# Kernel optimization log

Hardware: AMD Instinct MI355X
Metric: run time of the kernel (lower is better)

The kernel has to match this reference:

```python
import jax, jax.numpy as jnp
import numpy as np

D_MODEL = 1024
D_STATE = 16
D_CONV = 4
EXPAND = 2
D_INNER = D_MODEL * EXPAND
LN_EPS = 1e-5


def setup_inputs() -> dict:
    key = jax.random.key(0)
    ks = jax.random.split(key, 12)
    s = lambda fan_in: 1.0 / np.sqrt(fan_in)
    return {
        "x": jax.random.normal(ks[0], (4, 2048, D_MODEL), dtype=jnp.float32),
        "ln_w": jnp.ones((D_MODEL,), jnp.float32),
        "ln_b": jnp.zeros((D_MODEL,), jnp.float32),
        "W_in": jax.random.uniform(ks[1], (D_MODEL, 2 * D_INNER), jnp.float32, -s(D_MODEL), s(D_MODEL)),
        "b_in": jax.random.uniform(ks[2], (2 * D_INNER,), jnp.float32, -s(D_MODEL), s(D_MODEL)),
        "conv_w": jax.random.uniform(ks[3], (D_INNER, 1, D_CONV), jnp.float32, -s(D_CONV), s(D_CONV)),
        "conv_b": jax.random.uniform(ks[4], (D_INNER,), jnp.float32, -s(D_CONV), s(D_CONV)),
        "A_log": jax.random.normal(ks[5], (D_INNER, D_STATE), jnp.float32),
        "D": jax.random.normal(ks[6], (D_INNER,), jnp.float32),
        "W_x": jax.random.uniform(ks[7], (D_INNER, 2 * D_STATE), jnp.float32, -s(D_INNER), s(D_INNER)),
        "b_x": jax.random.uniform(ks[8], (2 * D_STATE,), jnp.float32, -s(D_INNER), s(D_INNER)),
        "W_out": jax.random.uniform(ks[9], (D_INNER, D_MODEL), jnp.float32, -s(D_INNER), s(D_INNER)),
        "b_out": jax.random.uniform(ks[10], (D_MODEL,), jnp.float32, -s(D_INNER), s(D_INNER)),
    }


def _selective_scan(xc, deltaA, Bm, Cm):
    # xc: (b, s, di), deltaA: (di, n), Bm/Cm: (b, s, n)
    b, _, di = xc.shape
    n = Bm.shape[-1]
    h0 = jnp.zeros((b, di, n), xc.dtype)

    def step(h, inp):
        xt, bt, ct = inp  # (b,di), (b,n), (b,n)
        h = deltaA[None] * h + xt[:, :, None] * bt[:, None, :]
        y = jnp.einsum('bin,bn->bi', h, ct)
        return h, y

    xs = (jnp.swapaxes(xc, 0, 1), jnp.swapaxes(Bm, 0, 1), jnp.swapaxes(Cm, 0, 1))
    _, ys = jax.lax.scan(step, h0, xs)  # ys: (s, b, di)
    return jnp.swapaxes(ys, 0, 1)


def reference(x, ln_w, ln_b, W_in, b_in, conv_w, conv_b, A_log, D, W_x, b_x, W_out, b_out):
    residual = x
    mu = jnp.mean(x, -1, keepdims=True)
    var = jnp.mean((x - mu) ** 2, -1, keepdims=True)
    xn = (x - mu) * jax.lax.rsqrt(var + LN_EPS) * ln_w + ln_b
    xg = xn @ W_in + b_in
    x_main, gate = jnp.split(xg, 2, axis=-1)  # (b,s,di) each
    # causal depthwise conv1d (left pad d_conv-1 == torch pad both + slice [:s])
    xt = jnp.swapaxes(x_main, 1, 2)  # (b, di, s)
    xc = jax.lax.conv_general_dilated(
        xt, conv_w, window_strides=(1,), padding=[(D_CONV - 1, 0)],
        feature_group_count=D_INNER, dimension_numbers=('NCH', 'OIH', 'NCH'))
    xc = xc + conv_b[None, :, None]
    x_conv = jax.nn.silu(jnp.swapaxes(xc, 1, 2))  # (b,s,di)
    ssm = x_conv @ W_x + b_x
    Bm, Cm = jnp.split(ssm, 2, axis=-1)  # (b,s,n)
    deltaA = jnp.exp(-jnp.exp(A_log))  # exp(A), A = -exp(A_log)
    y = _selective_scan(x_conv, deltaA, Bm, Cm)
    y = y + x_conv * D[None, None, :]
    y = y * jax.nn.silu(gate)
    out = y @ W_out + b_out
    return out + residual
```

## Files before the change

kernel.cpp:

```cpp
#include <hip/hip_runtime.h>
#include <stdint.h>

typedef unsigned short u16;
typedef short bf16x8 __attribute__((ext_vector_type(8)));
typedef float f32x4 __attribute__((ext_vector_type(4)));

#define TOKENS 8192
#define SEQ 2048
#define DM 1024
#define DI 2048
#define NCH 32
#define CLEN 64

__device__ __forceinline__ float bf2f(u16 u) {
  union { uint32_t i; float f; } v; v.i = ((uint32_t)u) << 16; return v.f;
}
__device__ __forceinline__ u16 f2bf(float f) {
  union { float f; uint32_t i; } v; v.f = f;
  uint32_t r = v.i + 0x7FFFu + ((v.i >> 16) & 1u);
  return (u16)(r >> 16);
}

__device__ __forceinline__ void g2lds16(const void* g, void* l) {
  __builtin_amdgcn_global_load_lds(
      (const __attribute__((address_space(1))) uint32_t*)g,
      (__attribute__((address_space(3))) uint32_t*)l, 16, 0, 0);
}

__global__ __launch_bounds__(256)
void transpose_to_bf16(const float* __restrict__ src, u16* __restrict__ dst,
                       int R, int C) {
  __shared__ float tile[64][65];
  const int i = threadIdx.x;
  const int tilesC = C >> 6;
  const int br = blockIdx.x / tilesC, bc = blockIdx.x % tilesC;
  const int r0 = br << 6, c0 = bc << 6;
  const int cx = (i & 15) << 2, ry = i >> 4;
#pragma unroll
  for (int p = 0; p < 4; ++p) {
    int row = ry + p * 16;
    float4 v = *(const float4*)&src[(size_t)(r0 + row) * C + c0 + cx];
    tile[row][cx + 0] = v.x; tile[row][cx + 1] = v.y;
    tile[row][cx + 2] = v.z; tile[row][cx + 3] = v.w;
  }
  __syncthreads();
#pragma unroll
  for (int p = 0; p < 4; ++p) {
    int cr = ry + p * 16;
    ushort4 o;
    o.x = f2bf(tile[cx + 0][cr]); o.y = f2bf(tile[cx + 1][cr]);
    o.z = f2bf(tile[cx + 2][cr]); o.w = f2bf(tile[cx + 3][cr]);
    *(ushort4*)&dst[(size_t)(c0 + cr) * R + r0 + cx] = o;
  }
}

__global__ __launch_bounds__(256)
void txpose_wx(const float* __restrict__ src, u16* __restrict__ dst) {
  const int gid = blockIdx.x * 256 + threadIdx.x;
  const int k = gid >> 5, n = gid & 31;
  dst[(size_t)n * DI + k] = f2bf(src[gid]);
}

__global__ __launch_bounds__(256)
void layernorm_bf16(const float* __restrict__ x, const float* __restrict__ lw,
                    const float* __restrict__ lb, u16* __restrict__ xn) {
  const int row = blockIdx.x, tid = threadIdx.x;
  const float4 v = *(const float4*)&x[(size_t)row * DM + tid * 4];
  float s = v.x + v.y + v.z + v.w;
  float q = v.x * v.x + v.y * v.y + v.z * v.z + v.w * v.w;
#pragma unroll
  for (int m = 1; m < 64; m <<= 1) { s += __shfl_xor(s, m); q += __shfl_xor(q, m); }
  __shared__ float red[8];
  const int w = tid >> 6, lane = tid & 63;
  if (lane == 0) { red[w] = s; red[4 + w] = q; }
  __syncthreads();
  s = red[0] + red[1] + red[2] + red[3];
  q = red[4] + red[5] + red[6] + red[7];
  const float mu = s * (1.f / DM);
  const float var = q * (1.f / DM) - mu * mu;
  const float rs = rsqrtf(var + 1e-5f);
  const float4 wv = *(const float4*)&lw[tid * 4];
  const float4 bv = *(const float4*)&lb[tid * 4];
  ushort4 o;
  o.x = f2bf((v.x - mu) * rs * wv.x + bv.x);
  o.y = f2bf((v.y - mu) * rs * wv.y + bv.y);
  o.z = f2bf((v.z - mu) * rs * wv.z + bv.z);
  o.w = f2bf((v.w - mu) * rs * wv.w + bv.w);
  *(ushort4*)&xn[(size_t)row * DM + tid * 4] = o;
}

#define TILE256 (2 * 256 * 64)
__global__ __launch_bounds__(512, 2)
void gemm_256(const u16* __restrict__ A, const u16* __restrict__ Bt,
              const float* __restrict__ bias, u16* __restrict__ out,
              int M, int N, int K) {
  __shared__ __align__(16) u16 lds[2 * TILE256];
  const int tid = threadIdx.x, wid = tid >> 6, lane = tid & 63;
  const int ntiles = N >> 8;
  int bid = blockIdx.x;
  {
    const int cpx = gridDim.x >> 3;
    bid = (bid & 7) * cpx + (bid >> 3);
  }
  const int tm = bid / ntiles, tn = bid % ntiles;
  const int m0 = tm << 8, n0 = tn << 8;
  const int wm = (wid >> 2) * 128, wn = (wid & 3) * 64;
  const int fr = lane & 15, fg = lane >> 4;
  const int c0 = (fg ^ (fr & 7)) << 4;
  const int NK = K >> 6;

  f32x4 acc[8][4];
#pragma unroll
  for (int mi = 0; mi < 8; ++mi)
#pragma unroll
    for (int ni = 0; ni < 4; ++ni) acc[mi][ni] = (f32x4){0.f, 0.f, 0.f, 0.f};

  auto stage = [&](int T) {
    const int kt = T << 6;
    u16* buf = lds + (T & 1) * TILE256;
#pragma unroll
    for (int i = 0; i < 4; ++i) {
      const int s = i * 512 + tid;
      const int row = s >> 3, l = (s & 7) ^ (row & 7);
      g2lds16(A + (size_t)(m0 + row) * K + kt + l * 8, buf + s * 8);
    }
    u16* bufB = buf + 256 * 64;
#pragma unroll
    for (int i = 0; i < 4; ++i) {
      const int s = i * 512 + tid;
      const int row = s >> 3, l = (s & 7) ^ (row & 7);
      g2lds16(Bt + (size_t)(n0 + row) * K + kt + l * 8, bufB + s * 8);
    }
  };

  stage(0); stage(1);
  asm volatile("s_waitcnt vmcnt(8)" ::: "memory");
  __builtin_amdgcn_s_barrier();
  asm volatile("" ::: "memory");

  for (int T = 0; T < NK; ++T) {
    const char* bufA = (const char*)(lds + (T & 1) * TILE256);
    const char* bufB = bufA + 256 * 64 * 2;
#pragma unroll
    for (int ks = 0; ks < 2; ++ks) {
      const int cb = c0 ^ (ks << 6);
      bf16x8 af[8], bfr[4];
#pragma unroll
      for (int ni = 0; ni < 4; ++ni)
        bfr[ni] = *(const bf16x8*)(bufB + (wn + ni * 16 + fr) * 128 + cb);
#pragma unroll
      for (int mi = 0; mi < 8; ++mi)
        af[mi] = *(const bf16x8*)(bufA + (wm + mi * 16 + fr) * 128 + cb);
      __builtin_amdgcn_s_setprio(1);
#pragma unroll
      for (int mi = 0; mi < 8; ++mi)
#pragma unroll
        for (int ni = 0; ni < 4; ++ni)
          acc[mi][ni] = __builtin_amdgcn_mfma_f32_16x16x32_bf16(
              af[mi], bfr[ni], acc[mi][ni], 0, 0, 0);
      __builtin_amdgcn_s_setprio(0);
    }
    __builtin_amdgcn_s_barrier();
    asm volatile("" ::: "memory");
    if (T + 2 < NK) {
      stage(T + 2);
      asm volatile("s_waitcnt vmcnt(8)" ::: "memory");
    } else if (T + 1 < NK) {
      asm volatile("s_waitcnt vmcnt(0)" ::: "memory");
    }
    __builtin_amdgcn_s_barrier();
    asm volatile("" ::: "memory");
  }

#pragma unroll
  for (int mi = 0; mi < 8; ++mi)
#pragma unroll
    for (int ni = 0; ni < 4; ++ni) {
      const int col = n0 + wn + ni * 16 + fr;
      const float bcol = bias[col];
#pragma unroll
      for (int j = 0; j < 4; ++j) {
        const int row = m0 + wm + mi * 16 + fg * 4 + j;
        out[(size_t)row * N + col] = f2bf(acc[mi][ni][j] + bcol);
      }
    }
}

#define TILE_U16 ((128 + 256) * 64)
template <int EPI>
__global__ __launch_bounds__(512, 1)
void gemm3(const u16* __restrict__ A, const u16* __restrict__ Bt,
           const float* __restrict__ bias, const float* __restrict__ resid,
           void* __restrict__ out, int M, int N, int K) {
  __shared__ __align__(16) u16 lds[3 * TILE_U16];
  const int tid = threadIdx.x, wid = tid >> 6, lane = tid & 63;
  const int ntiles = N >> 8;
  int bid = blockIdx.x;
  {
    const int cpx = gridDim.x >> 3;
    bid = (bid & 7) * cpx + (bid >> 3);
  }
  const int tm = bid / ntiles, tn = bid % ntiles;
  const int m0 = tm << 7, n0 = tn << 8;
  const int wm = (wid >> 2) * 64, wn = (wid & 3) * 64;
  const int fr = lane & 15, fg = lane >> 4;
  const int c0 = (fg ^ (fr & 7)) << 4;
  const int NK = K >> 6;

  f32x4 acc[4][4];
#pragma unroll
  for (int mi = 0; mi < 4; ++mi)
#pragma unroll
    for (int ni = 0; ni < 4; ++ni) acc[mi][ni] = (f32x4){0.f, 0.f, 0.f, 0.f};

  auto stage = [&](int T) {
    const int kt = T << 6;
    u16* buf = lds + (T % 3) * TILE_U16;
#pragma unroll
    for (int i = 0; i < 2; ++i) {
      const int s = i * 512 + tid;
      const int row = s >> 3, l = (s & 7) ^ (row & 7);
      g2lds16(A + (size_t)(m0 + row) * K + kt + l * 8, buf + s * 8);
    }
    u16* bufB = buf + 128 * 64;
#pragma unroll
    for (int i = 0; i < 4; ++i) {
      const int s = i * 512 + tid;
      const int row = s >> 3, l = (s & 7) ^ (row & 7);
      g2lds16(Bt + (size_t)(n0 + row) * K + kt + l * 8, bufB + s * 8);
    }
  };

  stage(0); stage(1); stage(2);
  asm volatile("s_waitcnt vmcnt(12)" ::: "memory");
  __builtin_amdgcn_s_barrier();
  asm volatile("" ::: "memory");

  for (int T = 0; T < NK; ++T) {
    const char* bufA = (const char*)(lds + (T % 3) * TILE_U16);
    const char* bufB = bufA + 128 * 64 * 2;
    bf16x8 af[2][4], bf_[2][4];
#pragma unroll
    for (int ks = 0; ks < 2; ++ks) {
      const int cb = c0 ^ (ks << 6);
#pragma unroll
      for (int mi = 0; mi < 4; ++mi)
        af[ks][mi] = *(const bf16x8*)(bufA + (wm + mi * 16 + fr) * 128 + cb);
#pragma unroll
      for (int ni = 0; ni < 4; ++ni)
        bf_[ks][ni] = *(const bf16x8*)(bufB + (wn + ni * 16 + fr) * 128 + cb);
    }
    __builtin_amdgcn_s_setprio(1);
#pragma unroll
    for (int ks = 0; ks < 2; ++ks)
#pragma unroll
      for (int mi = 0; mi < 4; ++mi)
#pragma unroll
        for (int ni = 0; ni < 4; ++ni)
          acc[mi][ni] = __builtin_amdgcn_mfma_f32_16x16x32_bf16(
              af[ks][mi], bf_[ks][ni], acc[mi][ni], 0, 0, 0);
    __builtin_amdgcn_s_setprio(0);
    __builtin_amdgcn_s_barrier();
    asm volatile("" ::: "memory");
    if (T + 3 < NK) {
      stage(T + 3);
      asm volatile("s_waitcnt vmcnt(12)" ::: "memory");
    } else if (T + 2 < NK) {
      asm volatile("s_waitcnt vmcnt(6)" ::: "memory");
    } else if (T + 1 < NK) {
      asm volatile("s_waitcnt vmcnt(0)" ::: "memory");
    }
    __builtin_amdgcn_s_barrier();
    asm volatile("" ::: "memory");
  }

#pragma unroll
  for (int mi = 0; mi < 4; ++mi)
#pragma unroll
    for (int ni = 0; ni < 4; ++ni) {
      const int col = n0 + wn + ni * 16 + fr;
      const float bcol = bias[col];
#pragma unroll
      for (int j = 0; j < 4; ++j) {
        const int row = m0 + wm + mi * 16 + fg * 4 + j;
        float v = acc[mi][ni][j] + bcol;
        if (EPI == 1) {
          ((float*)out)[(size_t)row * N + col] = v + resid[(size_t)row * N + col];
        } else {
          ((u16*)out)[(size_t)row * N + col] = f2bf(v);
        }
      }
    }
}

__global__ __launch_bounds__(256)
void conv_silu(const u16* __restrict__ xg, const float* __restrict__ cw,
               const float* __restrict__ cb, u16* __restrict__ xconv) {
  const int t = blockIdx.x;
  const int s = t & (SEQ - 1);
  const int d = threadIdx.x * 8;
  float xv[4][8];
#pragma unroll
  for (int j = 0; j < 4; ++j) {
    const int ss = s - 3 + j;
    if (ss >= 0) {
      uint4 u = *(const uint4*)&xg[(size_t)(t - 3 + j) * (2 * DI) + d];
      const u16* pu = (const u16*)&u;
#pragma unroll
      for (int q = 0; q < 8; ++q) xv[j][q] = bf2f(pu[q]);
    } else {
#pragma unroll
      for (int q = 0; q < 8; ++q) xv[j][q] = 0.f;
    }
  }
  u16 outp[8];
#pragma unroll
  for (int q = 0; q < 8; ++q) {
    const float4 wq = *(const float4*)&cw[(d + q) * 4];
    float a = cb[d + q] + wq.x * xv[0][q] + wq.y * xv[1][q] + wq.z * xv[2][q] +
              wq.w * xv[3][q];
    outp[q] = f2bf(a / (1.f + __expf(-a)));
  }
  *(uint4*)&xconv[(size_t)t * DI + d] = *(const uint4*)outp;
}

__global__ __launch_bounds__(256)
void bc_gemm(const u16* __restrict__ xconv, const u16* __restrict__ wxT,
             float* __restrict__ BCp) {
  __shared__ __align__(16) u16 As[128 * 64];
  __shared__ __align__(16) u16 Bs[32 * 64];
  const int tid = threadIdx.x, w = tid >> 6, lane = tid & 63;
  const int mt = blockIdx.x & 63;
  const int ks_id = blockIdx.x >> 6;
  const int m0 = mt << 7;
  const int k0 = ks_id << 9;
  const int fr = lane & 15, fg = lane >> 4;
  f32x4 acc[2][2];
#pragma unroll
  for (int mf = 0; mf < 2; ++mf)
#pragma unroll
    for (int nf = 0; nf < 2; ++nf) acc[mf][nf] = (f32x4){0.f, 0.f, 0.f, 0.f};

  for (int kt = k0; kt < k0 + 512; kt += 64) {
#pragma unroll
    for (int i = 0; i < 4; ++i) {
      int ch = w * 64 + lane + i * 256;
      int row = ch >> 3, c16 = ch & 7;
      g2lds16(xconv + (size_t)(m0 + row) * DI + kt + c16 * 8,
              (u16*)As + (size_t)(w * 64 + i * 256) * 8);
    }
    {
      int row = tid >> 3, c16 = tid & 7;
      g2lds16(wxT + (size_t)row * DI + kt + c16 * 8,
              (u16*)Bs + (size_t)(w * 64) * 8);
    }
    __syncthreads();
#pragma unroll
    for (int ks = 0; ks < 2; ++ks) {
      bf16x8 af[2], bfr[2];
#pragma unroll
      for (int mf = 0; mf < 2; ++mf)
        af[mf] = *(const bf16x8*)&As[(w * 32 + mf * 16 + fr) * 64 + ks * 32 + fg * 8];
#pragma unroll
      for (int nf = 0; nf < 2; ++nf)
        bfr[nf] = *(const bf16x8*)&Bs[(nf * 16 + fr) * 64 + ks * 32 + fg * 8];
#pragma unroll
      for (int mf = 0; mf < 2; ++mf)
#pragma unroll
        for (int nf = 0; nf < 2; ++nf)
          acc[mf][nf] = __builtin_amdgcn_mfma_f32_16x16x32_bf16(
              af[mf], bfr[nf], acc[mf][nf], 0, 0, 0);
    }
    __syncthreads();
  }
#pragma unroll
  for (int mf = 0; mf < 2; ++mf)
#pragma unroll
    for (int nf = 0; nf < 2; ++nf) {
      const int col = nf * 16 + fr;
#pragma unroll
      for (int j = 0; j < 4; ++j) {
        const int row = m0 + w * 32 + mf * 16 + fg * 4 + j;
        BCp[((size_t)ks_id * TOKENS + row) * 32 + col] = acc[mf][nf][j];
      }
    }
}

__global__ __launch_bounds__(256)
void bc_reduce(const float* __restrict__ BCp, const float* __restrict__ bx,
               float* __restrict__ BC) {
  const int gid = blockIdx.x * 256 + threadIdx.x;
  const int c = gid & 31;
  const size_t t = gid >> 5;
  float s = bx[c] + BCp[t * 32 + c] + BCp[((size_t)TOKENS + t) * 32 + c] +
            BCp[((size_t)2 * TOKENS + t) * 32 + c] +
            BCp[((size_t)3 * TOKENS + t) * 32 + c];
  const int dc = (c < 16) ? 2 * c : 2 * (c - 16) + 1;
  BC[t * 32 + dc] = s;
}

__global__ __launch_bounds__(256)
void scan_passA(const u16* __restrict__ xconv, const float* __restrict__ BC,
                const float* __restrict__ A_log, float* __restrict__ F) {
  __shared__ float bcs[CLEN * 32];
  const int blk = blockIdx.x;
  const int j = blk & (NCH - 1);
  const int dg = (blk >> 5) & 7;
  const int b = blk >> 8;
  const int tid = threadIdx.x;
  const int d = dg * 256 + tid;
  const int t0 = j * CLEN;
  {
    const float4* s4 = (const float4*)(BC + (size_t)(b * SEQ + t0) * 32);
    float4* d4 = (float4*)bcs;
#pragma unroll
    for (int i = 0; i < 2; ++i) d4[tid + i * 256] = s4[tid + i * 256];
  }
  float dA[16], h[16];
#pragma unroll
  for (int n = 0; n < 16; ++n) {
    dA[n] = __expf(-__expf(A_log[d * 16 + n]));
    h[n] = 0.f;
  }
  __syncthreads();
  const u16* xcp = xconv + (size_t)(b * SEQ + t0) * DI + d;
  for (int t = 0; t < CLEN; ++t) {
    const float xc = bf2f(*xcp);
    xcp += DI;
#pragma unroll
    for (int n = 0; n < 16; ++n)
      h[n] = fmaf(dA[n], h[n], xc * bcs[t * 32 + 2 * n]);
  }
  float* fp = F + ((size_t)((b * NCH + j) * DI) + d) * 16;
#pragma unroll
  for (int n = 0; n < 16; n += 4) {
    float4 v = {h[n], h[n + 1], h[n + 2], h[n + 3]};
    *(float4*)&fp[n] = v;
  }
}

__global__ __launch_bounds__(256)
void scan_passB(const float* __restrict__ A_log, float* __restrict__ F) {
  const int gid = blockIdx.x * 256 + threadIdx.x;
  const int n = gid & 15;
  const int d = (gid >> 4) & (DI - 1);
  const int b = gid >> 15;
  const float dAL = __expf(-(float)CLEN * __expf(A_log[d * 16 + n]));
  float carry = 0.f;
  const size_t base = ((size_t)(b * NCH) * DI + d) * 16 + n;
  const size_t stride = (size_t)DI * 16;
  for (int j = 0; j < NCH; ++j) {
    const size_t idx = base + (size_t)j * stride;
    const float f = F[idx];
    F[idx] = carry;
    carry = fmaf(dAL, carry, f);
  }
}

__global__ __launch_bounds__(256)
void scan_passC(const u16* __restrict__ xconv, const u16* __restrict__ xg,
                const float* __restrict__ BC, const float* __restrict__ A_log,
                const float* __restrict__ Dv, const float* __restrict__ F,
                u16* __restrict__ yact) {
  __shared__ float bcs[CLEN * 32];
  const int blk = blockIdx.x;
  const int j = blk & (NCH - 1);
  const int dg = (blk >> 5) & 7;
  const int b = blk >> 8;
  const int tid = threadIdx.x;
  const int d = dg * 256 + tid;
  const int t0 = j * CLEN;
  {
    const float4* s4 = (const float4*)(BC + (size_t)(b * SEQ + t0) * 32);
    float4* d4 = (float4*)bcs;
#pragma unroll
    for (int i = 0; i < 2; ++i) d4[tid + i * 256] = s4[tid + i * 256];
  }
  float dA[16], h[16];
  const float* fp = F + ((size_t)((b * NCH + j) * DI) + d) * 16;
#pragma unroll
  for (int n = 0; n < 16; n += 4) {
    float4 v = *(const float4*)&fp[n];
    h[n] = v.x; h[n + 1] = v.y; h[n + 2] = v.z; h[n + 3] = v.w;
  }
#pragma unroll
  for (int n = 0; n < 16; ++n) dA[n] = __expf(-__expf(A_log[d * 16 + n]));
  const float Dd = Dv[d];
  __syncthreads();
  const u16* xcp = xconv + (size_t)(b * SEQ + t0) * DI + d;
  const u16* gp = xg + (size_t)(b * SEQ + t0) * (2 * DI) + DI + d;
  u16* yp = yact + (size_t)(b * SEQ + t0) * DI + d;
  for (int t = 0; t < CLEN; ++t) {
    const float xc = bf2f(*xcp);
    const float g = bf2f(*gp);
    float y0 = 0.f, y1 = 0.f, y2 = 0.f, y3 = 0.f;
#pragma unroll
    for (int n = 0; n < 16; n += 4) {
      h[n]     = fmaf(dA[n],     h[n],     xc * bcs[t * 32 + 2 * n]);
      y0 = fmaf(bcs[t * 32 + 2 * n + 1], h[n], y0);
      h[n + 1] = fmaf(dA[n + 1], h[n + 1], xc * bcs[t * 32 + 2 * n + 2]);
      y1 = fmaf(bcs[t * 32 + 2 * n + 3], h[n + 1], y1);
      h[n + 2] = fmaf(dA[n + 2], h[n + 2], xc * bcs[t * 32 + 2 * n + 4]);
      y2 = fmaf(bcs[t * 32 + 2 * n + 5], h[n + 2], y2);
      h[n + 3] = fmaf(dA[n + 3], h[n + 3], xc * bcs[t * 32 + 2 * n + 6]);
      y3 = fmaf(bcs[t * 32 + 2 * n + 7], h[n + 3], y3);
    }
    const float y = (y0 + y1) + (y2 + y3);
    const float ya = (y + xc * Dd) * (g / (1.f + __expf(-g)));
    *yp = f2bf(ya);
    xcp += DI; gp += 2 * DI; yp += DI;
  }
}

extern "C" void kernel_launch(void* const* d_in, const int* in_sizes, int n_in,
                              void* d_out, int out_size, void* d_ws, size_t ws_size,
                              hipStream_t stream) {
  const float* x     = (const float*)d_in[0];
  const float* ln_w  = (const float*)d_in[1];
  const float* ln_b  = (const float*)d_in[2];
  const float* W_in  = (const float*)d_in[3];
  const float* b_in  = (const float*)d_in[4];
  const float* cw    = (const float*)d_in[5];
  const float* cb    = (const float*)d_in[6];
  const float* A_log = (const float*)d_in[7];
  const float* Dv    = (const float*)d_in[8];
  const float* W_x   = (const float*)d_in[9];
  const float* b_x   = (const float*)d_in[10];
  const float* W_out = (const float*)d_in[11];
  const float* b_out = (const float*)d_in[12];

  char* ws = (char*)d_ws;
  size_t off = 0;
  auto alloc = [&](size_t bytes) {
    void* p = ws + off;
    off += (bytes + 255) & ~(size_t)255;
    return p;
  };
  u16* WinT  = (u16*)alloc((size_t)(2 * DI) * DM * 2);
  u16* WoutT = (u16*)alloc((size_t)DM * DI * 2);
  u16* xn    = (u16*)alloc((size_t)TOKENS * DM * 2);
  u16* xg    = (u16*)alloc((size_t)TOKENS * (2 * DI) * 2);
  u16* xconv = (u16*)alloc((size_t)TOKENS * DI * 2);
  float* BC  = (float*)alloc((size_t)TOKENS * 32 * 4);
  u16* yact  = (u16*)alloc((size_t)TOKENS * DI * 2);
  u16* WxT   = (u16*)alloc((size_t)32 * DI * 2);
  float* BCp = (float*)alloc((size_t)4 * TOKENS * 32 * 4);
  float* F   = (float*)xn;
  (void)ws_size; (void)in_sizes; (void)n_in; (void)out_size;

  transpose_to_bf16<<<(DM / 64) * ((2 * DI) / 64), 256, 0, stream>>>(W_in, WinT, DM, 2 * DI);
  transpose_to_bf16<<<(DI / 64) * (DM / 64), 256, 0, stream>>>(W_out, WoutT, DI, DM);
  txpose_wx<<<(DI * 32) / 256, 256, 0, stream>>>(W_x, WxT);
  layernorm_bf16<<<TOKENS, 256, 0, stream>>>(x, ln_w, ln_b, xn);
  gemm_256<<<(TOKENS / 256) * ((2 * DI) / 256), 512, 0, stream>>>(
      xn, WinT, b_in, xg, TOKENS, 2 * DI, DM);
  conv_silu<<<TOKENS, 256, 0, stream>>>(xg, cw, cb, xconv);
  bc_gemm<<<256, 256, 0, stream>>>(xconv, WxT, BCp);
  bc_reduce<<<(TOKENS * 32) / 256, 256, 0, stream>>>(BCp, b_x, BC);
  scan_passA<<<4 * 8 * NCH, 256, 0, stream>>>(xconv, BC, A_log, F);
  scan_passB<<<512, 256, 0, stream>>>(A_log, F);
  scan_passC<<<4 * 8 * NCH, 256, 0, stream>>>(xconv, xg, BC, A_log, Dv, F, yact);
  gemm3<1><<<(TOKENS / 128) * (DM / 256), 512, 0, stream>>>(
      yact, WoutT, b_out, x, d_out, TOKENS, DM, DI);
}
```

Baseline: 394.2 us.

## Interleave GEMM tile loads with MFMA phases and de-interleave B/C layout for scans

The in-projection GEMM main loop is split into four sub-phases per K tile. Each phase issues a slice of the next tiles' global-to-LDS loads, so memory traffic is spread across the MFMA work instead of arriving in bursts, and B-fragments are held for the whole tile. The B/C projection buffer is also stored contiguous (B then C) instead of interleaved, so the scan kernels can read B and C with float4 LDS loads. The risks are more barriers per tile, delicate vmcnt accounting, and higher register pressure.

```diff
diff --git a/kernel.cpp b/kernel.cpp
--- a/kernel.cpp
+++ b/kernel.cpp
@@ -91,9 +91,9 @@
 
 #define TILE256 (2 * 256 * 64)
 __global__ __launch_bounds__(512, 2)
-void gemm_256(const u16* __restrict__ A, const u16* __restrict__ Bt,
-              const float* __restrict__ bias, u16* __restrict__ out,
-              int M, int N, int K) {
+void gemm8(const u16* __restrict__ A, const u16* __restrict__ Bt,
+           const float* __restrict__ bias, u16* __restrict__ out,
+           int M, int N, int K) {
   __shared__ __align__(16) u16 lds[2 * TILE256];
   const int tid = threadIdx.x, wid = tid >> 6, lane = tid & 63;
   const int ntiles = N >> 8;
@@ -115,61 +115,82 @@
 #pragma unroll
     for (int ni = 0; ni < 4; ++ni) acc[mi][ni] = (f32x4){0.f, 0.f, 0.f, 0.f};
 
-  auto stage = [&](int T) {
+  auto stage_unit = [&](int T, int isB, int u) {
     const int kt = T << 6;
-    u16* buf = lds + (T & 1) * TILE256;
-#pragma unroll
-    for (int i = 0; i < 4; ++i) {
-      const int s = i * 512 + tid;
-      const int row = s >> 3, l = (s & 7) ^ (row & 7);
-      g2lds16(A + (size_t)(m0 + row) * K + kt + l * 8, buf + s * 8);
-    }
-    u16* bufB = buf + 256 * 64;
-#pragma unroll
-    for (int i = 0; i < 4; ++i) {
-      const int s = i * 512 + tid;
-      const int row = s >> 3, l = (s & 7) ^ (row & 7);
-      g2lds16(Bt + (size_t)(n0 + row) * K + kt + l * 8, bufB + s * 8);
-    }
+    const int row = u * 64 + (tid >> 3);
+    const int l = (tid & 7) ^ (row & 7);
+    const u16* src = (isB ? Bt + (size_t)(n0 + row) * K
+                          : A + (size_t)(m0 + row) * K) + kt + l * 8;
+    g2lds16(src, lds + (size_t)(T & 1) * TILE256 + isB * 16384 + u * 4096 + tid * 8);
   };
 
-  stage(0); stage(1);
-  asm volatile("s_waitcnt vmcnt(8)" ::: "memory");
+#pragma unroll
+  for (int u = 0; u < 4; ++u) stage_unit(0, 1, u);
+#pragma unroll
+  for (int u = 0; u < 4; ++u) stage_unit(0, 0, u);
+#pragma unroll
+  for (int u = 0; u < 4; ++u) stage_unit(1, 1, u);
+  stage_unit(1, 0, 0); stage_unit(1, 0, 2);
+  asm volatile("s_waitcnt vmcnt(6)" ::: "memory");
   __builtin_amdgcn_s_barrier();
   asm volatile("" ::: "memory");
 
-  for (int T = 0; T < NK; ++T) {
-    const char* bufA = (const char*)(lds + (T & 1) * TILE256);
-    const char* bufB = bufA + 256 * 64 * 2;
-#pragma unroll
-    for (int ks = 0; ks < 2; ++ks) {
-      const int cb = c0 ^ (ks << 6);
-      bf16x8 af[8], bfr[4];
-#pragma unroll
-      for (int ni = 0; ni < 4; ++ni)
-        bfr[ni] = *(const bf16x8*)(bufB + (wn + ni * 16 + fr) * 128 + cb);
-#pragma unroll
-      for (int mi = 0; mi < 8; ++mi)
-        af[mi] = *(const bf16x8*)(bufA + (wm + mi * 16 + fr) * 128 + cb);
+  bf16x8 bfr[2][4];
+  for (int t = 0; t < NK; ++t) {
+    const char* bufA = (const char*)(lds + (t & 1) * TILE256);
+    const char* bufB = bufA + 32768;
+#pragma unroll
+    for (int q = 0; q < 4; ++q) {
+      bf16x8 af[2][2];
+      if (q == 0) {
+#pragma unroll
+        for (int ks = 0; ks < 2; ++ks) {
+          const int cb = c0 ^ (ks << 6);
+#pragma unroll
+          for (int ni = 0; ni < 4; ++ni)
+            bfr[ks][ni] = *(const bf16x8*)(bufB + (wn + ni * 16 + fr) * 128 + cb);
+        }
+      }
+#pragma unroll
+      for (int ks = 0; ks < 2; ++ks) {
+        const int cb = c0 ^ (ks << 6);
+#pragma unroll
+        for (int r = 0; r < 2; ++r)
+          af[ks][r] = *(const bf16x8*)(bufA + (wm + (2 * q + r) * 16 + fr) * 128 + cb);
+      }
+      if (q == 0) {
+        if (t + 1 < NK) { stage_unit(t + 1, 0, 1); stage_unit(t + 1, 0, 3); }
+      } else if (q == 1) {
+        if (t + 2 < NK) { stage_unit(t + 2, 1, 0); stage_unit(t + 2, 1, 1); }
+      } else if (q == 2) {
+        if (t + 2 < NK) { stage_unit(t + 2, 1, 2); stage_unit(t + 2, 1, 3); }
+      } else {
+        if (t + 2 < NK) { stage_unit(t + 2, 0, 0); stage_unit(t + 2, 0, 2); }
+      }
+      __builtin_amdgcn_sched_barrier(0);
+      __builtin_amdgcn_s_barrier();
+      asm volatile("s_waitcnt lgkmcnt(0)" ::: "memory");
+      __builtin_amdgcn_sched_barrier(0);
       __builtin_amdgcn_s_setprio(1);
 #pragma unroll
-      for (int mi = 0; mi < 8; ++mi)
-#pragma unroll
-        for (int ni = 0; ni < 4; ++ni)
-          acc[mi][ni] = __builtin_amdgcn_mfma_f32_16x16x32_bf16(
-              af[mi], bfr[ni], acc[mi][ni], 0, 0, 0);
+      for (int ks = 0; ks < 2; ++ks)
+#pragma unroll
+        for (int r = 0; r < 2; ++r)
+#pragma unroll
+          for (int ni = 0; ni < 4; ++ni)
+            acc[2 * q + r][ni] = __builtin_amdgcn_mfma_f32_16x16x32_bf16(
+                af[ks][r], bfr[ks][ni], acc[2 * q + r][ni], 0, 0, 0);
       __builtin_amdgcn_s_setprio(0);
-    }
-    __builtin_amdgcn_s_barrier();
-    asm volatile("" ::: "memory");
-    if (T + 2 < NK) {
-      stage(T + 2);
-      asm volatile("s_waitcnt vmcnt(8)" ::: "memory");
-    } else if (T + 1 < NK) {
-      asm volatile("s_waitcnt vmcnt(0)" ::: "memory");
-    }
-    __builtin_amdgcn_s_barrier();
-    asm volatile("" ::: "memory");
+      if (q == 3) {
+        if (t + 2 < NK) {
+          asm volatile("s_waitcnt vmcnt(6)" ::: "memory");
+        } else if (t + 1 < NK) {
+          asm volatile("s_waitcnt vmcnt(0)" ::: "memory");
+        }
+      }
+      __builtin_amdgcn_s_barrier();
+      asm volatile("" ::: "memory");
+    }
   }
 
 #pragma unroll
@@ -395,8 +416,7 @@
   float s = bx[c] + BCp[t * 32 + c] + BCp[((size_t)TOKENS + t) * 32 + c] +
             BCp[((size_t)2 * TOKENS + t) * 32 + c] +
             BCp[((size_t)3 * TOKENS + t) * 32 + c];
-  const int dc = (c < 16) ? 2 * c : 2 * (c - 16) + 1;
-  BC[t * 32 + dc] = s;
+  BC[t * 32 + c] = s;
 }
 
 __global__ __launch_bounds__(256)
@@ -427,9 +447,15 @@
   for (int t = 0; t < CLEN; ++t) {
     const float xc = bf2f(*xcp);
     xcp += DI;
-#pragma unroll
-    for (int n = 0; n < 16; ++n)
-      h[n] = fmaf(dA[n], h[n], xc * bcs[t * 32 + 2 * n]);
+    const float* bt = &bcs[t * 32];
+#pragma unroll
+    for (int n4 = 0; n4 < 4; ++n4) {
+      const float4 bv = *(const float4*)&bt[n4 * 4];
+      h[4 * n4 + 0] = fmaf(dA[4 * n4 + 0], h[4 * n4 + 0], xc * bv.x);
+      h[4 * n4 + 1] = fmaf(dA[4 * n4 + 1], h[4 * n4 + 1], xc * bv.y);
+      h[4 * n4 + 2] = fmaf(dA[4 * n4 + 2], h[4 * n4 + 2], xc * bv.z);
+      h[4 * n4 + 3] = fmaf(dA[4 * n4 + 3], h[4 * n4 + 3], xc * bv.w);
+    }
   }
   float* fp = F + ((size_t)((b * NCH + j) * DI) + d) * 16;
 #pragma unroll
@@ -493,17 +519,21 @@
   for (int t = 0; t < CLEN; ++t) {
     const float xc = bf2f(*xcp);
     const float g = bf2f(*gp);
+    const float* bt = &bcs[t * 32];
     float y0 = 0.f, y1 = 0.f, y2 = 0.f, y3 = 0.f;
 #pragma unroll
-    for (int n = 0; n < 16; n += 4) {
-      h[n]     = fmaf(dA[n],     h[n],     xc * bcs[t * 32 + 2 * n]);
-      y0 = fmaf(bcs[t * 32 + 2 * n + 1], h[n], y0);
-      h[n + 1] = fmaf(dA[n + 1], h[n + 1], xc * bcs[t * 32 + 2 * n + 2]);
-      y1 = fmaf(bcs[t * 32 + 2 * n + 3], h[n + 1], y1);
-      h[n + 2] = fmaf(dA[n + 2], h[n + 2], xc * bcs[t * 32 + 2 * n + 4]);
-      y2 = fmaf(bcs[t * 32 + 2 * n + 5], h[n + 2], y2);
-      h[n + 3] = fmaf(dA[n + 3], h[n + 3], xc * bcs[t * 32 + 2 * n + 6]);
-      y3 = fmaf(bcs[t * 32 + 2 * n + 7], h[n + 3], y3);
+    for (int n4 = 0; n4 < 4; ++n4) {
+      const float4 bv = *(const float4*)&bt[n4 * 4];
+      const float4 cv = *(const float4*)&bt[16 + n4 * 4];
+      const int n = 4 * n4;
+      h[n]     = fmaf(dA[n],     h[n],     xc * bv.x);
+      y0 = fmaf(cv.x, h[n], y0);
+      h[n + 1] = fmaf(dA[n + 1], h[n + 1], xc * bv.y);
+      y1 = fmaf(cv.y, h[n + 1], y1);
+      h[n + 2] = fmaf(dA[n + 2], h[n + 2], xc * bv.z);
+      y2 = fmaf(cv.z, h[n + 2], y2);
+      h[n + 3] = fmaf(dA[n + 3], h[n + 3], xc * bv.w);
+      y3 = fmaf(cv.w, h[n + 3], y3);
     }
     const float y = (y0 + y1) + (y2 + y3);
     const float ya = (y + xc * Dd) * (g / (1.f + __expf(-g)));
@@ -552,7 +582,7 @@
   transpose_to_bf16<<<(DI / 64) * (DM / 64), 256, 0, stream>>>(W_out, WoutT, DI, DM);
   txpose_wx<<<(DI * 32) / 256, 256, 0, stream>>>(W_x, WxT);
   layernorm_bf16<<<TOKENS, 256, 0, stream>>>(x, ln_w, ln_b, xn);
-  gemm_256<<<(TOKENS / 256) * ((2 * DI) / 256), 512, 0, stream>>>(
+  gemm8<<<(TOKENS / 256) * ((2 * DI) / 256), 512, 0, stream>>>(
       xn, WinT, b_in, xg, TOKENS, 2 * DI, DM);
   conv_silu<<<TOKENS, 256, 0, stream>>>(xg, cw, cb, xconv);
   bc_gemm<<<256, 256, 0, stream>>>(xconv, WxT, BCp);
```

Result: faster. 383.2 us (-2.8%).
